# Performance work log

Measured on AMD Instinct MI355X. Metric: run time of the kernel, lower is better.

The kernel has to match this reference:

```python
import jax, jax.numpy as jnp
import numpy as np

N_NODES = 50000
N_EDGES = 800000
IN_DIM = 128
HID = 128
OUT_DIM = 64
NUM_GRAPHS = 512
GM_P = 2.0
EPS = 1e-6


def setup_inputs() -> dict:
    key = jax.random.key(0)
    ks = jax.random.split(key, 12)
    x = jax.random.normal(ks[0], (N_NODES, IN_DIM), dtype=jnp.float32)
    edge_index = jax.random.randint(ks[1], (2, N_EDGES), 0, N_NODES, dtype=jnp.int64)
    batch = jnp.sort(jax.random.randint(ks[2], (N_NODES,), 0, NUM_GRAPHS, dtype=jnp.int64))
    def lin(k, fan_in, fan_out):
        w = jax.random.normal(k, (fan_in, fan_out), dtype=jnp.float32) / np.sqrt(fan_in)
        return w
    return {
        "x": x,
        "edge_index": edge_index,
        "batch": batch,
        # 3 GCN conv layers (weight + bias each)
        "W0": lin(ks[3], IN_DIM, HID), "b0": jnp.zeros((HID,), jnp.float32),
        "W1": lin(ks[4], HID, HID),    "b1": jnp.zeros((HID,), jnp.float32),
        "W2": lin(ks[5], HID, HID),    "b2": jnp.zeros((HID,), jnp.float32),
        # 2 FF layers: [HID->HID], [HID->OUT_DIM]
        "Wf0": lin(ks[6], HID, HID),   "bf0": jnp.zeros((HID,), jnp.float32),
        "Wf1": lin(ks[7], HID, OUT_DIM), "bf1": jnp.zeros((OUT_DIM,), jnp.float32),
    }


def _gcn_layer(h, src, dst, deg_inv_sqrt, W, b):
    # PyG GCNConv: h' = D^-1/2 (A + I) D^-1/2 (h W) + b, deg includes self-loop
    h = h @ W                                           # [N, F]
    norm = deg_inv_sqrt[src] * deg_inv_sqrt[dst]        # [E]
    msg = h[src] * norm[:, None]                        # gather + scale, [E, F]
    agg = jax.ops.segment_sum(msg, dst, num_segments=N_NODES)
    agg = agg + h * (deg_inv_sqrt * deg_inv_sqrt)[:, None]   # self-loop term (norm = 1/deg)
    return agg + b


def _gm_pool(x, batch, p):
    # sign-preserving generalized mean pool via scatter_mean
    xt = jnp.sign(x) * (jnp.abs(x) + EPS) ** p
    sums = jax.ops.segment_sum(xt, batch, num_segments=NUM_GRAPHS)
    cnt = jax.ops.segment_sum(jnp.ones((x.shape[0],), x.dtype), batch, num_segments=NUM_GRAPHS)
    pooled = sums / jnp.maximum(cnt, 1.0)[:, None]
    return jnp.sign(pooled) * (jnp.abs(pooled) + EPS) ** (1.0 / p)


def reference(x, edge_index, batch, W0, b0, W1, b1, W2, b2, Wf0, bf0, Wf1, bf1):
    src, dst = edge_index[0], edge_index[1]
    # degree of aggregation targets, with +1 for self-loops (computed once; graph is static)
    deg = jax.ops.segment_sum(jnp.ones((N_EDGES,), x.dtype), dst, num_segments=N_NODES) + 1.0
    deg_inv_sqrt = jax.lax.rsqrt(deg)

    h = _gcn_layer(x, src, dst, deg_inv_sqrt, W0, b0)
    h = jax.nn.relu(h)
    h = _gcn_layer(h, src, dst, deg_inv_sqrt, W1, b1)
    h = jax.nn.relu(h)
    h = _gcn_layer(h, src, dst, deg_inv_sqrt, W2, b2)  # no relu after last conv

    graph_repr = _gm_pool(h, batch, GM_P)              # [G, HID]
    graph_repr = jax.nn.relu(graph_repr)

    z = jax.nn.relu(graph_repr @ Wf0 + bf0)
    logits = z @ Wf1 + bf1                             # [G, OUT_DIM]
    return logits
```

## Files before the change

kernel.cpp:

```cpp
#include <hip/hip_runtime.h>

#define N_NODES   50000
#define M_PAD     50048
#define N_TILES   1564
#define GEMM_GRID 782
#define N_EDGES   800000
#define HID       128
#define OUT_DIM   64
#define NUM_GRAPHS 512
#define EPS       1e-6f
#define NBUCK     196
#define BUCKCAP   6144
#define ABLOCKS   98

typedef __attribute__((ext_vector_type(8))) short short8;
typedef __attribute__((ext_vector_type(16))) float f32x16;

static __device__ __forceinline__ unsigned short f2bf(float f) {
    unsigned u = __builtin_bit_cast(unsigned, f);
    u += 0x7FFFu + ((u >> 16) & 1u);
    return (unsigned short)(u >> 16);
}
static __device__ __forceinline__ float bf2f(unsigned short h) {
    unsigned u = ((unsigned)h) << 16;
    return __builtin_bit_cast(float, u);
}

static __device__ __forceinline__ float signpow(float x, bool sqrt_mode) {
    if (x == 0.0f) return 0.0f;
    float a = fabsf(x) + EPS;
    float v = sqrt_mode ? sqrtf(a) : a * a;
    return x > 0.0f ? v : -v;
}

__global__ __launch_bounds__(256) void k_bucketize(const int* __restrict__ ei,
                                                   int* __restrict__ gcnt,
                                                   unsigned* __restrict__ ebuf) {
    __shared__ int lcnt[NBUCK];
    __shared__ int lbase[NBUCK];
    int tid = threadIdx.x;
    for (int i = tid; i < NBUCK; i += 256) lcnt[i] = 0;
    __syncthreads();

    const uint4* src4 = (const uint4*)ei;
    const uint4* dst4 = (const uint4*)(ei + N_EDGES);
    int base4 = blockIdx.x * 2048;

    #pragma unroll 1
    for (int it = 0; it < 8; it++) {
        int i4 = base4 + it * 256 + tid;
        if (i4 < N_EDGES / 4) {
            uint4 d = dst4[i4];
            atomicAdd(&lcnt[d.x >> 8], 1);
            atomicAdd(&lcnt[d.y >> 8], 1);
            atomicAdd(&lcnt[d.z >> 8], 1);
            atomicAdd(&lcnt[d.w >> 8], 1);
        }
    }
    __syncthreads();
    for (int i = tid; i < NBUCK; i += 256) {
        lbase[i] = atomicAdd(&gcnt[i], lcnt[i]);
        lcnt[i] = 0;
    }
    __syncthreads();

    #pragma unroll 1
    for (int it = 0; it < 8; it++) {
        int i4 = base4 + it * 256 + tid;
        if (i4 < N_EDGES / 4) {
            uint4 d = dst4[i4];
            uint4 s = src4[i4];
            unsigned dd[4] = {d.x, d.y, d.z, d.w};
            unsigned ss[4] = {s.x, s.y, s.z, s.w};
            #pragma unroll
            for (int k = 0; k < 4; k++) {
                int b = dd[k] >> 8;
                int p = atomicAdd(&lcnt[b], 1);
                ebuf[(size_t)b * BUCKCAP + lbase[b] + p] = ss[k] | (dd[k] << 16);
            }
        }
    }
}

__global__ __launch_bounds__(256) void k_csr(const unsigned* __restrict__ ebuf,
                                             const int* __restrict__ gcnt,
                                             int* __restrict__ offs,
                                             float* __restrict__ dis,
                                             int* __restrict__ csr) {
    __shared__ int cntA[256];
    __shared__ int scanA[256];
    __shared__ int sbase;
    int b = blockIdx.x;
    int t = threadIdx.x;
    int n0 = b * 256;

    int v = (t < NBUCK) ? gcnt[t] : 0;
    scanA[t] = v;
    __syncthreads();
    for (int off = 1; off < 256; off <<= 1) {
        int u = (t >= off) ? scanA[t - off] : 0;
        __syncthreads();
        scanA[t] += u;
        __syncthreads();
    }
    if (t == 0) sbase = (b == 0) ? 0 : scanA[b - 1];
    __syncthreads();
    int base  = sbase;
    int count = gcnt[b];
    const unsigned* eb = ebuf + (size_t)b * BUCKCAP;

    cntA[t] = 0;
    __syncthreads();
    for (int i = t; i < count; i += 256)
        atomicAdd(&cntA[eb[i] >> 16 & 0xFF], 1);
    __syncthreads();
    int c = cntA[t];
    scanA[t] = c;
    __syncthreads();
    for (int off = 1; off < 256; off <<= 1) {
        int u = (t >= off) ? scanA[t - off] : 0;
        __syncthreads();
        scanA[t] += u;
        __syncthreads();
    }
    int excl = scanA[t] - c;
    int n = n0 + t;
    if (n < N_NODES) {
        offs[n] = base + excl;
        dis[n]  = rsqrtf((float)c + 1.0f);
    }
    if (b == 0 && t == 0) offs[N_NODES] = N_EDGES;
    scanA[t] = excl;
    cntA[t] = 0;
    __syncthreads();
    for (int i = t; i < count; i += 256) {
        unsigned vv = eb[i];
        int ln = (vv >> 16) & 0xFF;
        int p = atomicAdd(&cntA[ln], 1);
        csr[base + scanA[ln] + p] = (int)(vv & 0xFFFFu);
    }
}

__global__ void k_wsplit3(const float* __restrict__ W0, const float* __restrict__ W1,
                          const float* __restrict__ W2, short* __restrict__ Wth,
                          short* __restrict__ Wtl) {
    int which = blockIdx.y;
    const float* W = which == 0 ? W0 : (which == 1 ? W1 : W2);
    int tid = blockIdx.x * blockDim.x + threadIdx.x;
    int k = tid & 127, n = tid >> 7;
    float w = W[k * HID + n];
    unsigned short h = f2bf(w);
    Wth[which * HID * HID + n * HID + k] = (short)h;
    Wtl[which * HID * HID + n * HID + k] = (short)f2bf(w - bf2f(h));
}

template<int FP32SRC>
__global__ __launch_bounds__(256) void k_gemm_mfma(const void* __restrict__ Asrc_h,
                                                   const void* __restrict__ Asrc_l,
                                                   const short* __restrict__ Wh,
                                                   const short* __restrict__ Wl,
                                                   unsigned short* __restrict__ th,
                                                   const float* __restrict__ scale) {
    __shared__ short As_h[32 * 128];
    __shared__ short As_l[32 * 128];
    int tid  = threadIdx.x;
    int lane = tid & 63;
    int col  = (tid >> 6) * 32 + (lane & 31);
    int kh   = lane >> 5;
    int r    = lane & 31;

    short8 bh[8], bl[8];
    #pragma unroll
    for (int ks = 0; ks < 8; ks++) {
        bh[ks] = *(const short8*)(Wh + (size_t)col * HID + ks * 16 + kh * 8);
        bl[ks] = *(const short8*)(Wl + (size_t)col * HID + ks * 16 + kh * 8);
    }

    int su0 = tid, su1 = tid + 256;
    int sr0 = su0 >> 4, sc0 = su0 & 15;
    int sr1 = su1 >> 4, sc1 = su1 & 15;
    int sw0 = sr0 * 128 + ((sc0 ^ (sr0 & 7)) * 8);
    int sw1 = sr1 * 128 + ((sc1 ^ (sr1 & 7)) * 8);

    for (int tile = blockIdx.x; tile < N_TILES; tile += GEMM_GRID) {
        int row0 = tile * 32;
        __syncthreads();
        if (FP32SRC) {
            const float* gx = (const float*)Asrc_h;
            #pragma unroll
            for (int u = 0; u < 2; u++) {
                int sr = u ? sr1 : sr0, sc = u ? sc1 : sc0, sw = u ? sw1 : sw0;
                int gr = row0 + sr; if (gr >= N_NODES) gr = N_NODES - 1;
                const float* src = gx + (size_t)gr * HID + sc * 8;
                float4 a = ((const float4*)src)[0];
                float4 b = ((const float4*)src)[1];
                float vals[8] = {a.x, a.y, a.z, a.w, b.x, b.y, b.z, b.w};
                short8 hi, lo;
                #pragma unroll
                for (int j = 0; j < 8; j++) {
                    unsigned short hh = f2bf(vals[j]);
                    hi[j] = (short)hh;
                    lo[j] = (short)f2bf(vals[j] - bf2f(hh));
                }
                *(short8*)&As_h[sw] = hi;
                *(short8*)&As_l[sw] = lo;
            }
        } else {
            const short* gh = (const short*)Asrc_h + (size_t)row0 * HID;
            const short* gl = (const short*)Asrc_l + (size_t)row0 * HID;
            *(short8*)&As_h[sw0] = *(const short8*)(gh + sr0 * HID + sc0 * 8);
            *(short8*)&As_h[sw1] = *(const short8*)(gh + sr1 * HID + sc1 * 8);
            *(short8*)&As_l[sw0] = *(const short8*)(gl + sr0 * HID + sc0 * 8);
            *(short8*)&As_l[sw1] = *(const short8*)(gl + sr1 * HID + sc1 * 8);
        }
        __syncthreads();

        short8 ah[8], al[8];
        #pragma unroll
        for (int ks = 0; ks < 8; ks++) {
            int cg = ks * 2 + kh;
            int off = r * 128 + ((cg ^ (r & 7)) * 8);
            ah[ks] = *(const short8*)&As_h[off];
            al[ks] = *(const short8*)&As_l[off];
        }

        f32x16 acc = {0.f};
        #pragma unroll
        for (int ks = 0; ks < 8; ks++) {
            acc = __builtin_amdgcn_mfma_f32_32x32x16_bf16(ah[ks], bh[ks], acc, 0, 0, 0);
            acc = __builtin_amdgcn_mfma_f32_32x32x16_bf16(al[ks], bh[ks], acc, 0, 0, 0);
            acc = __builtin_amdgcn_mfma_f32_32x32x16_bf16(ah[ks], bl[ks], acc, 0, 0, 0);
        }

        #pragma unroll
        for (int reg = 0; reg < 16; reg++) {
            int row = row0 + (reg & 3) + 8 * (reg >> 2) + 4 * kh;
            float v = acc[reg] * scale[row];
            th[(size_t)row * HID + col] = f2bf(v);
        }
    }
}

__global__ __launch_bounds__(256) void k_agg(const unsigned short* __restrict__ th,
                                             const int* __restrict__ offs,
                                             const int* __restrict__ csr_src,
                                             const float* __restrict__ dis,
                                             const float* __restrict__ bias,
                                             float* __restrict__ hout,
                                             short* __restrict__ hh,
                                             short* __restrict__ hl,
                                             int mode) {
    int node = blockIdx.x * 4 + (threadIdx.x >> 6);
    if (node >= N_NODES) return;
    int lane = threadIdx.x & 63;
    int c  = lane & 31;
    int e  = lane >> 5;
    int beg = offs[node], end = offs[node + 1];
    float dn = dis[node];

    float ax[4] = {}, ay[4] = {}, az[4] = {}, aw[4] = {};
    for (int j = beg; j < end; j += 8) {
        #pragma unroll
        for (int k = 0; k < 4; k++) {
            int jj = j + k * 2 + e;
            int jc = jj < end ? jj : end - 1;
            int s = csr_src[jc];
            float m = (jj < end) ? 1.0f : 0.0f;
            uint2 v = *(const uint2*)&th[(size_t)s * HID + c * 4];
            float v0 = __builtin_bit_cast(float, v.x << 16);
            float v1 = __builtin_bit_cast(float, v.x & 0xFFFF0000u);
            float v2 = __builtin_bit_cast(float, v.y << 16);
            float v3 = __builtin_bit_cast(float, v.y & 0xFFFF0000u);
            ax[k] = fmaf(v0, m, ax[k]);
            ay[k] = fmaf(v1, m, ay[k]);
            az[k] = fmaf(v2, m, az[k]);
            aw[k] = fmaf(v3, m, aw[k]);
        }
    }
    float tx = (ax[0] + ax[1]) + (ax[2] + ax[3]);
    float ty = (ay[0] + ay[1]) + (ay[2] + ay[3]);
    float tz = (az[0] + az[1]) + (az[2] + az[3]);
    float tw = (aw[0] + aw[1]) + (aw[2] + aw[3]);
    tx += __shfl_xor(tx, 32);
    ty += __shfl_xor(ty, 32);
    tz += __shfl_xor(tz, 32);
    tw += __shfl_xor(tw, 32);

    if (e == 0) {
        ushort4 sh = *(const ushort4*)&th[(size_t)node * HID + c * 4];
        float4 b4  = *(const float4*)&bias[c * 4];
        float ox = (tx + bf2f(sh.x)) * dn + b4.x;
        float oy = (ty + bf2f(sh.y)) * dn + b4.y;
        float oz = (tz + bf2f(sh.z)) * dn + b4.z;
        float ow = (tw + bf2f(sh.w)) * dn + b4.w;
        if (mode == 1) {
            ox = fmaxf(ox, 0.f); oy = fmaxf(oy, 0.f);
            oz = fmaxf(oz, 0.f); ow = fmaxf(ow, 0.f);
            unsigned short hx = f2bf(ox), hy = f2bf(oy), hz = f2bf(oz), hw = f2bf(ow);
            ushort4 vh; vh.x = hx; vh.y = hy; vh.z = hz; vh.w = hw;
            ushort4 vl;
            vl.x = f2bf(ox - bf2f(hx)); vl.y = f2bf(oy - bf2f(hy));
            vl.z = f2bf(oz - bf2f(hz)); vl.w = f2bf(ow - bf2f(hw));
            *(ushort4*)&hh[(size_t)node * HID + c * 4] = vh;
            *(ushort4*)&hl[(size_t)node * HID + c * 4] = vl;
        } else {
            float4 o = make_float4(ox, oy, oz, ow);
            *(float4*)&hout[(size_t)node * HID + c * 4] = o;
        }
    }
}

__global__ __launch_bounds__(256) void k_poolff(const float* __restrict__ h,
                                                const int* __restrict__ batch,
                                                const float* __restrict__ Wf0,
                                                const float* __restrict__ bf0,
                                                const float* __restrict__ Wf1,
                                                const float* __restrict__ bf1,
                                                float* __restrict__ out) {
    __shared__ float smx[4][64], smy[4][64];
    __shared__ float row[128], zrow[128];
    __shared__ int bnd[2];
    int g = blockIdx.x;
    int t = threadIdx.x;
    if (t < 2) {
        int target = g + t;
        int lo = 0, hi = N_NODES;
        while (lo < hi) {
            int mid = (lo + hi) >> 1;
            if (batch[mid] < target) lo = mid + 1; else hi = mid;
        }
        bnd[t] = lo;
    }
    __syncthreads();
    int beg = bnd[0], end = bnd[1];

    int c = t & 63, slot = t >> 6;
    float sx = 0.f, sy = 0.f;
    for (int n = beg + slot; n < end; n += 4) {
        float2 v = *(const float2*)&h[(size_t)n * HID + c * 2];
        sx += signpow(v.x, false);
        sy += signpow(v.y, false);
    }
    smx[slot][c] = sx; smy[slot][c] = sy;
    __syncthreads();
    if (slot == 0) {
        sx = (smx[0][c] + smx[1][c]) + (smx[2][c] + smx[3][c]);
        sy = (smy[0][c] + smy[1][c]) + (smy[2][c] + smy[3][c]);
        float cnt = fmaxf((float)(end - beg), 1.0f);
        row[c * 2]     = fmaxf(signpow(sx / cnt, true), 0.f);
        row[c * 2 + 1] = fmaxf(signpow(sy / cnt, true), 0.f);
    }
    __syncthreads();
    if (t < 128) {
        float acc = bf0[t];
        #pragma unroll 8
        for (int k = 0; k < 128; k++) acc = fmaf(row[k], Wf0[k * 128 + t], acc);
        zrow[t] = fmaxf(acc, 0.f);
    }
    __syncthreads();
    if (t < OUT_DIM) {
        float a2 = bf1[t];
        #pragma unroll 8
        for (int k = 0; k < 128; k++) a2 = fmaf(zrow[k], Wf1[k * OUT_DIM + t], a2);
        out[g * OUT_DIM + t] = a2;
    }
}

static inline size_t align256(size_t x) { return (x + 255) & ~(size_t)255; }

extern "C" void kernel_launch(void* const* d_in, const int* in_sizes, int n_in,
                              void* d_out, int out_size, void* d_ws, size_t ws_size,
                              hipStream_t stream) {
    const float* x     = (const float*)d_in[0];
    const int*   ei    = (const int*)d_in[1];
    const int*   batch = (const int*)d_in[2];
    const float* W0  = (const float*)d_in[3];  const float* b0  = (const float*)d_in[4];
    const float* W1  = (const float*)d_in[5];  const float* b1  = (const float*)d_in[6];
    const float* W2  = (const float*)d_in[7];  const float* b2  = (const float*)d_in[8];
    const float* Wf0 = (const float*)d_in[9];  const float* bf0 = (const float*)d_in[10];
    const float* Wf1 = (const float*)d_in[11]; const float* bf1 = (const float*)d_in[12];
    float* out = (float*)d_out;

    char* p = (char*)d_ws;
    unsigned short* th = (unsigned short*)p; p += align256((size_t)M_PAD * HID * 2);
    short* bufAh = (short*)p; p += align256((size_t)M_PAD * HID * 2);
    short* bufAl = (short*)p; p += align256((size_t)M_PAD * HID * 2);
    short* bufBh = (short*)p; p += align256((size_t)M_PAD * HID * 2);
    short* bufBl = (short*)p; p += align256((size_t)M_PAD * HID * 2);
    float* h     = (float*)bufBh;
    unsigned* ebuf = (unsigned*)p; p += align256((size_t)NBUCK * BUCKCAP * 4);
    int*   gcnt    = (int*)p;   p += align256((size_t)NBUCK * 4);
    int*   offs    = (int*)p;   p += align256((size_t)(N_NODES + 1) * 4);
    int*   csr     = (int*)p;   p += align256((size_t)N_EDGES * 4);
    float* dis     = (float*)p; p += align256((size_t)N_NODES * 4);
    short* Wth     = (short*)p; p += align256((size_t)3 * HID * HID * 2);
    short* Wtl     = (short*)p; p += align256((size_t)3 * HID * HID * 2);

    hipMemsetAsync(gcnt, 0, (size_t)NBUCK * 4, stream);

    k_bucketize<<<ABLOCKS, 256, 0, stream>>>(ei, gcnt, ebuf);
    k_csr      <<<NBUCK, 256, 0, stream>>>(ebuf, gcnt, offs, dis, csr);

    dim3 wg(64, 3);
    k_wsplit3<<<wg, 256, 0, stream>>>(W0, W1, W2, Wth, Wtl);

    int agg_blocks = (N_NODES + 3) / 4;

    k_gemm_mfma<1><<<GEMM_GRID, 256, 0, stream>>>(x, nullptr, Wth, Wtl, th, dis);
    k_agg<<<agg_blocks, 256, 0, stream>>>(th, offs, csr, dis, b0,
                                          nullptr, bufBh, bufBl, 1);
    k_gemm_mfma<0><<<GEMM_GRID, 256, 0, stream>>>(bufBh, bufBl,
                                                  Wth + HID * HID, Wtl + HID * HID, th, dis);
    k_agg<<<agg_blocks, 256, 0, stream>>>(th, offs, csr, dis, b1,
                                          nullptr, bufAh, bufAl, 1);
    k_gemm_mfma<0><<<GEMM_GRID, 256, 0, stream>>>(bufAh, bufAl,
                                                  Wth + 2 * HID * HID, Wtl + 2 * HID * HID, th, dis);
    k_agg<<<agg_blocks, 256, 0, stream>>>(th, offs, csr, dis, b2,
                                          h, nullptr, nullptr, 0);

    k_poolff<<<NUM_GRAPHS, 256, 0, stream>>>(h, batch, Wf0, bf0, Wf1, bf1, out);
}
```

Measured before the change: 206.3 us.

## Store hidden features in 16-column slices and aggregate one slice per block

Intermediate node features move from row-major [N,128] to eight column slices of [N,16]. The GEMM writes and reads this layout, and pooling reads it. The aggregation kernel now gives each block one slice and eight nodes, so a gathered neighbour row is a contiguous 32-byte segment. The aim is to shrink the per-slice working set for better L2 hit rates on the random gathers. The cost is that CSR indices and offsets are re-read once per slice, and there are 8x more, lighter aggregation blocks.

Result: slower. 322.7 us (+56.4%).

```diff
diff --git a/kernel.cpp b/kernel.cpp
--- a/kernel.cpp
+++ b/kernel.cpp
@@ -12,6 +12,7 @@
 #define NBUCK     196
 #define BUCKCAP   6144
 #define ABLOCKS   98
+#define SS        (M_PAD * 16)
 
 typedef __attribute__((ext_vector_type(8))) short short8;
 typedef __attribute__((ext_vector_type(16))) float f32x16;
@@ -181,6 +182,9 @@
     int sr1 = su1 >> 4, sc1 = su1 & 15;
     int sw0 = sr0 * 128 + ((sc0 ^ (sr0 & 7)) * 8);
     int sw1 = sr1 * 128 + ((sc1 ^ (sr1 & 7)) * 8);
+
+    int oslice = col >> 4, oc16 = col & 15;
+    unsigned short* thp = th + (size_t)oslice * SS;
 
     for (int tile = blockIdx.x; tile < N_TILES; tile += GEMM_GRID) {
         int row0 = tile * 32;
@@ -206,12 +210,18 @@
                 *(short8*)&As_l[sw] = lo;
             }
         } else {
-            const short* gh = (const short*)Asrc_h + (size_t)row0 * HID;
-            const short* gl = (const short*)Asrc_l + (size_t)row0 * HID;
-            *(short8*)&As_h[sw0] = *(const short8*)(gh + sr0 * HID + sc0 * 8);
-            *(short8*)&As_h[sw1] = *(const short8*)(gh + sr1 * HID + sc1 * 8);
-            *(short8*)&As_l[sw0] = *(const short8*)(gl + sr0 * HID + sc0 * 8);
-            *(short8*)&As_l[sw1] = *(const short8*)(gl + sr1 * HID + sc1 * 8);
+            const short* gh = (const short*)Asrc_h;
+            const short* gl = (const short*)Asrc_l;
+            #pragma unroll
+            for (int u = 0; u < 2; u++) {
+                int uu = u ? (tid + 256) : tid;
+                int s = uu >> 6, rr = (uu >> 1) & 31, half = uu & 1;
+                int cg = s * 2 + half;
+                int sw = rr * 128 + ((cg ^ (rr & 7)) * 8);
+                size_t off = (size_t)s * SS + (size_t)(row0 + rr) * 16 + half * 8;
+                *(short8*)&As_h[sw] = *(const short8*)(gh + off);
+                *(short8*)&As_l[sw] = *(const short8*)(gl + off);
+            }
         }
         __syncthreads();
 
@@ -236,7 +246,7 @@
         for (int reg = 0; reg < 16; reg++) {
             int row = row0 + (reg & 3) + 8 * (reg >> 2) + 4 * kh;
             float v = acc[reg] * scale[row];
-            th[(size_t)row * HID + col] = f2bf(v);
+            thp[(size_t)row * 16 + oc16] = f2bf(v);
         }
     }
 }
@@ -250,62 +260,62 @@
                                              short* __restrict__ hh,
                                              short* __restrict__ hl,
                                              int mode) {
-    int node = blockIdx.x * 4 + (threadIdx.x >> 6);
+    int slice = blockIdx.x & 7;
+    int ng    = blockIdx.x >> 3;
+    int tid   = threadIdx.x;
+    int wave  = tid >> 6, lane = tid & 63;
+    int nhalf = lane >> 5;
+    int l32   = lane & 31;
+    int cg    = l32 & 3;
+    int e     = l32 >> 2;
+    int node  = ng * 8 + wave * 2 + nhalf;
     if (node >= N_NODES) return;
-    int lane = threadIdx.x & 63;
-    int c  = lane & 31;
-    int e  = lane >> 5;
+
     int beg = offs[node], end = offs[node + 1];
     float dn = dis[node];
-
-    float ax[4] = {}, ay[4] = {}, az[4] = {}, aw[4] = {};
+    const unsigned short* tb = th + (size_t)slice * SS;
+
+    float a0 = 0.f, a1 = 0.f, a2 = 0.f, a3 = 0.f;
     for (int j = beg; j < end; j += 8) {
-        #pragma unroll
-        for (int k = 0; k < 4; k++) {
-            int jj = j + k * 2 + e;
-            int jc = jj < end ? jj : end - 1;
-            int s = csr_src[jc];
-            float m = (jj < end) ? 1.0f : 0.0f;
-            uint2 v = *(const uint2*)&th[(size_t)s * HID + c * 4];
-            float v0 = __builtin_bit_cast(float, v.x << 16);
-            float v1 = __builtin_bit_cast(float, v.x & 0xFFFF0000u);
-            float v2 = __builtin_bit_cast(float, v.y << 16);
-            float v3 = __builtin_bit_cast(float, v.y & 0xFFFF0000u);
-            ax[k] = fmaf(v0, m, ax[k]);
-            ay[k] = fmaf(v1, m, ay[k]);
-            az[k] = fmaf(v2, m, az[k]);
-            aw[k] = fmaf(v3, m, aw[k]);
-        }
-    }
-    float tx = (ax[0] + ax[1]) + (ax[2] + ax[3]);
-    float ty = (ay[0] + ay[1]) + (ay[2] + ay[3]);
-    float tz = (az[0] + az[1]) + (az[2] + az[3]);
-    float tw = (aw[0] + aw[1]) + (aw[2] + aw[3]);
-    tx += __shfl_xor(tx, 32);
-    ty += __shfl_xor(ty, 32);
-    tz += __shfl_xor(tz, 32);
-    tw += __shfl_xor(tw, 32);
+        int jj = j + e;
+        int jc = jj < end ? jj : end - 1;
+        int s = csr_src[jc];
+        float m = (jj < end) ? 1.0f : 0.0f;
+        ushort4 v = *(const ushort4*)&tb[(size_t)s * 16 + cg * 4];
+        a0 = fmaf(bf2f(v.x), m, a0);
+        a1 = fmaf(bf2f(v.y), m, a1);
+        a2 = fmaf(bf2f(v.z), m, a2);
+        a3 = fmaf(bf2f(v.w), m, a3);
+    }
+    #pragma unroll
+    for (int msk = 4; msk <= 16; msk <<= 1) {
+        a0 += __shfl_xor(a0, msk);
+        a1 += __shfl_xor(a1, msk);
+        a2 += __shfl_xor(a2, msk);
+        a3 += __shfl_xor(a3, msk);
+    }
 
     if (e == 0) {
-        ushort4 sh = *(const ushort4*)&th[(size_t)node * HID + c * 4];
-        float4 b4  = *(const float4*)&bias[c * 4];
-        float ox = (tx + bf2f(sh.x)) * dn + b4.x;
-        float oy = (ty + bf2f(sh.y)) * dn + b4.y;
-        float oz = (tz + bf2f(sh.z)) * dn + b4.z;
-        float ow = (tw + bf2f(sh.w)) * dn + b4.w;
+        ushort4 sh = *(const ushort4*)&tb[(size_t)node * 16 + cg * 4];
+        float4 b4  = *(const float4*)&bias[slice * 16 + cg * 4];
+        float o0 = (a0 + bf2f(sh.x)) * dn + b4.x;
+        float o1 = (a1 + bf2f(sh.y)) * dn + b4.y;
+        float o2 = (a2 + bf2f(sh.z)) * dn + b4.z;
+        float o3 = (a3 + bf2f(sh.w)) * dn + b4.w;
+        size_t ob = (size_t)slice * SS + (size_t)node * 16 + cg * 4;
         if (mode == 1) {
-            ox = fmaxf(ox, 0.f); oy = fmaxf(oy, 0.f);
-            oz = fmaxf(oz, 0.f); ow = fmaxf(ow, 0.f);
-            unsigned short hx = f2bf(ox), hy = f2bf(oy), hz = f2bf(oz), hw = f2bf(ow);
-            ushort4 vh; vh.x = hx; vh.y = hy; vh.z = hz; vh.w = hw;
+            o0 = fmaxf(o0, 0.f); o1 = fmaxf(o1, 0.f);
+            o2 = fmaxf(o2, 0.f); o3 = fmaxf(o3, 0.f);
+            unsigned short h0 = f2bf(o0), h1 = f2bf(o1), h2 = f2bf(o2), h3 = f2bf(o3);
+            ushort4 vh; vh.x = h0; vh.y = h1; vh.z = h2; vh.w = h3;
             ushort4 vl;
-            vl.x = f2bf(ox - bf2f(hx)); vl.y = f2bf(oy - bf2f(hy));
-            vl.z = f2bf(oz - bf2f(hz)); vl.w = f2bf(ow - bf2f(hw));
-            *(ushort4*)&hh[(size_t)node * HID + c * 4] = vh;
-            *(ushort4*)&hl[(size_t)node * HID + c * 4] = vl;
+            vl.x = f2bf(o0 - bf2f(h0)); vl.y = f2bf(o1 - bf2f(h1));
+            vl.z = f2bf(o2 - bf2f(h2)); vl.w = f2bf(o3 - bf2f(h3));
+            *(ushort4*)&hh[ob] = vh;
+            *(ushort4*)&hl[ob] = vl;
         } else {
-            float4 o = make_float4(ox, oy, oz, ow);
-            *(float4*)&hout[(size_t)node * HID + c * 4] = o;
+            float4 o = make_float4(o0, o1, o2, o3);
+            *(float4*)&hout[ob] = o;
         }
     }
 }
@@ -335,9 +345,10 @@
     int beg = bnd[0], end = bnd[1];
 
     int c = t & 63, slot = t >> 6;
+    size_t sbase = (size_t)(c >> 3) * SS + (size_t)(c & 7) * 2;
     float sx = 0.f, sy = 0.f;
     for (int n = beg + slot; n < end; n += 4) {
-        float2 v = *(const float2*)&h[(size_t)n * HID + c * 2];
+        float2 v = *(const float2*)&h[sbase + (size_t)n * 16];
         sx += signpow(v.x, false);
         sy += signpow(v.y, false);
     }
@@ -404,7 +415,7 @@
     dim3 wg(64, 3);
     k_wsplit3<<<wg, 256, 0, stream>>>(W0, W1, W2, Wth, Wtl);
 
-    int agg_blocks = (N_NODES + 3) / 4;
+    int agg_blocks = (N_NODES / 8) * 8;
 
     k_gemm_mfma<1><<<GEMM_GRID, 256, 0, stream>>>(x, nullptr, Wth, Wtl, th, dis);
     k_agg<<<agg_blocks, 256, 0, stream>>>(th, offs, csr, dis, b0,
```
